# Performance work log

Measured on AMD Instinct MI355X. Metric: run time of the kernel, lower is better.

The kernel has to match this reference:

```python
import jax, jax.numpy as jnp
import numpy as np

B, V, F = 32, 1024, 16
A, P, NF = 32, 64, 128
C = P + A  # propagated feature width after concat with edge weights
D_OUT_IN = F + A + 2 * A * C  # 6192, input dim of output Dense


def setup_inputs() -> dict:
    key = jax.random.key(0)
    ks = jax.random.split(key, 4)
    return {
        "x": jax.random.normal(ks[0], (B, V, F), dtype=jnp.float32),
        "W_flr": jax.random.normal(ks[1], (F, P), dtype=jnp.float32) * (1.0 / np.sqrt(F)),
        "b_flr": jnp.zeros((P,), dtype=jnp.float32),
        "W_s": jax.random.normal(ks[2], (F, A), dtype=jnp.float32) * (1.0 / np.sqrt(F)),
        "b_s": jnp.zeros((A,), dtype=jnp.float32),
        "W_out": jax.random.normal(ks[3], (D_OUT_IN, NF), dtype=jnp.float32) * (1.0 / np.sqrt(D_OUT_IN)),
        "b_out": jnp.zeros((NF,), dtype=jnp.float32),
    }


def reference(x, W_flr, b_flr, W_s, b_s, W_out, b_out):
    # Per-vertex transforms
    feat = x @ W_flr + b_flr                      # (B,V,P)
    dist = x @ W_s + b_s                          # (B,V,A)
    ew = jnp.exp(-jnp.square(dist))               # (B,V,A) edge weights vertex->aggregator
    f = jnp.concatenate([feat, ew], axis=-1)      # (B,V,C)

    # Weighted broadcast then vertex-axis reduction (aggregator gather)
    w = jnp.transpose(ew, (0, 2, 1))              # (B,A,V)
    prod = w[..., None] * f[:, None, :, :]        # (B,A,V,C)
    agg_max = jnp.max(prod, axis=2)               # (B,A,C)
    agg_mean = jnp.mean(prod, axis=2)             # (B,A,C)
    agg = jnp.concatenate([agg_max, agg_mean], axis=-1)  # (B,A,2C)

    # Scatter aggregated features back to vertices, weighted by same edge weights
    upd = ew[..., None] * agg[:, None, :, :]      # (B,V,A,2C)
    upd = upd.reshape(B, V, A * 2 * C)            # (B,V,2AC)

    cat = jnp.concatenate([x, upd, ew], axis=-1)  # (B,V,F+2AC+A)
    return jnp.tanh(cat @ W_out + b_out)          # (B,V,NF)
```

## Files before the change

### kernel.cpp

```cpp
#include <hip/hip_runtime.h>
#include <hip/hip_bf16.h>
#include <math.h>

#define NB 32
#define NV 1024
#define NFT 16
#define NA 32
#define NP 64
#define NOUT 128
#define NC 96
#define NC2 192

#define NSPLIT 16
#define VPB 64

typedef __attribute__((ext_vector_type(8))) short bf16x8;
typedef __attribute__((ext_vector_type(4))) float f32x4;

__global__ __launch_bounds__(512, 2)
void k2p(const float* __restrict__ x,
         const float* __restrict__ W_flr,
         const float* __restrict__ b_flr,
         const float* __restrict__ W_s,
         const float* __restrict__ b_s,
         float* __restrict__ ewbuf,
         float* __restrict__ part) {
    __shared__ float xs[VPB][NFT];
    __shared__ float fs[VPB][NC];

    int b = blockIdx.x, vs = blockIdx.y, tid = threadIdx.x;
    int rowbase = b * NV + vs * VPB;

    if (tid < 256) {
        const float4* xsrc = (const float4*)(x + (size_t)rowbase * NFT);
        ((float4*)xs)[tid] = xsrc[tid];
    }
    __syncthreads();

    {
        int c  = tid & 127;
        int rh = tid >> 7;
        if (c < NC) {
            float Wcol[NFT], bias;
            if (c < NP) {
                bias = b_flr[c];
#pragma unroll
                for (int k = 0; k < NFT; ++k) Wcol[k] = W_flr[k * NP + c];
            } else {
                int a = c - NP;
                bias = b_s[a];
#pragma unroll
                for (int k = 0; k < NFT; ++k) Wcol[k] = W_s[k * NA + a];
            }
#pragma unroll
            for (int r0 = 0; r0 < 16; ++r0) {
                int r = rh * 16 + r0;
                float xr[NFT];
#pragma unroll
                for (int q = 0; q < 4; ++q)
                    ((float4*)xr)[q] = ((const float4*)xs[r])[q];
                float acc = bias;
#pragma unroll
                for (int k = 0; k < NFT; ++k)
                    acc = fmaf(xr[k], Wcol[k], acc);
                if (c >= NP) {
                    acc = __expf(-acc * acc);
                    ewbuf[(size_t)(rowbase + r) * NA + (c - NP)] = acc;
                }
                fs[r][c] = acc;
            }
        }
    }
    __syncthreads();

    int a  = tid >> 4;
    int c0 = (tid & 15) * 6;
    int ea = NP + a;

    float sm[6], mx[6];
#pragma unroll
    for (int j = 0; j < 6; ++j) { sm[j] = 0.f; mx[j] = -INFINITY; }

#pragma unroll 4
    for (int r = 0; r < VPB; ++r) {
        float e = fs[r][ea];
        float2 fA = *(const float2*)&fs[r][c0];
        float2 fB = *(const float2*)&fs[r][c0 + 2];
        float2 fC = *(const float2*)&fs[r][c0 + 4];
        float ff[6] = {fA.x, fA.y, fB.x, fB.y, fC.x, fC.y};
#pragma unroll
        for (int j = 0; j < 6; ++j) {
            float p = e * ff[j];
            sm[j] += p;
            mx[j] = fmaxf(mx[j], p);
        }
    }

    float* pb = part + (size_t)((b * NSPLIT + vs) * NA + a) * NC2;
#pragma unroll
    for (int q = 0; q < 3; ++q) {
        float2 vm = {mx[2 * q], mx[2 * q + 1]};
        float2 vsum = {sm[2 * q], sm[2 * q + 1]};
        *(float2*)&pb[c0 + 2 * q]      = vm;
        *(float2*)&pb[NC + c0 + 2 * q] = vsum;
    }
}

__global__ void k23(const float* __restrict__ part,
                    const float* __restrict__ W_out,
                    float* __restrict__ Gp) {
    __shared__ float aggL[NC2];
    int b = blockIdx.x, a = blockIdx.y, tid = threadIdx.x;

    {
        const float* pb = part + (size_t)(b * NSPLIT * NA + a) * NC2 + tid;
        const size_t stride = (size_t)NA * NC2;
        if (tid < NC) {
            float m = -INFINITY;
#pragma unroll
            for (int vsi = 0; vsi < NSPLIT; ++vsi)
                m = fmaxf(m, pb[vsi * stride]);
            aggL[tid] = m;
        } else {
            float s = 0.f;
#pragma unroll
            for (int vsi = 0; vsi < NSPLIT; ++vsi)
                s += pb[vsi * stride];
            aggL[tid] = s * (1.0f / (float)NV);
        }
    }
    __syncthreads();

    if (tid < NOUT) {
        int n = tid;
        const float* wr = W_out + (size_t)(NFT + a * NC2) * NOUT + n;
        float acc = W_out[(size_t)(NFT + NA * NC2 + a) * NOUT + n];
#pragma unroll 8
        for (int c = 0; c < NC2; ++c)
            acc = fmaf(aggL[c], wr[(size_t)c * NOUT], acc);
        Gp[(size_t)(b * NA + a) * NOUT + n] = acc;
    }
}

#define MB 64

__device__ inline void f2hl(float v, ushort& h, ushort& l) {
    __hip_bfloat16 hb = __float2bfloat16(v);
    float hf = __bfloat162float(hb);
    __hip_bfloat16 lb = __float2bfloat16(v - hf);
    h = *(ushort*)&hb;
    l = *(ushort*)&lb;
}

__global__ void k4_mfma(const float* __restrict__ x,
                        const float* __restrict__ ewbuf,
                        const float* __restrict__ Gp,
                        const float* __restrict__ W_out,
                        const float* __restrict__ b_out,
                        float* __restrict__ out) {
    __shared__ ushort BsH[1024 * 8];
    __shared__ ushort BsL[1024 * 8];
    __shared__ float  bs[NOUT];

    int rb = blockIdx.x;
    int b  = blockIdx.y;
    int tid = threadIdx.x;
    int rowbase = b * NV + rb * MB;

#pragma unroll
    for (int it = 0; it < 4; ++it) {
        int u = it * 256 + tid;
        int n = u & 127, koct = u >> 7;
        float v[8];
        if (koct < 2) {
#pragma unroll
            for (int j = 0; j < 8; ++j)
                v[j] = W_out[(size_t)(koct * 8 + j) * NOUT + n];
        } else if (koct < 6) {
#pragma unroll
            for (int j = 0; j < 8; ++j)
                v[j] = Gp[(size_t)b * NA * NOUT + (size_t)(koct * 8 + j - 16) * NOUT + n];
        } else {
#pragma unroll
            for (int j = 0; j < 8; ++j) v[j] = 0.f;
        }
        ushort h[8], l[8];
#pragma unroll
        for (int j = 0; j < 8; ++j) f2hl(v[j], h[j], l[j]);
        int cidx = ((koct >> 2) * 512) + ((n >> 4) * 64) + ((koct & 3) * 16) + (n & 15);
        *(bf16x8*)&BsH[cidx * 8] = *(bf16x8*)h;
        *(bf16x8*)&BsL[cidx * 8] = *(bf16x8*)l;
    }
    if (tid < NOUT) bs[tid] = b_out[tid];

    int w = tid >> 6, lane = tid & 63;
    int r16 = lane & 15, kg = lane >> 4;
    int arow = w * 16 + r16;
    int grow = rowbase + arow;

    float a0[8], a1[8];
    if (kg < 2) {
        *(float4*)&a0[0] = *(const float4*)&x[(size_t)grow * NFT + kg * 8];
        *(float4*)&a0[4] = *(const float4*)&x[(size_t)grow * NFT + kg * 8 + 4];
        *(float4*)&a1[0] = *(const float4*)&ewbuf[(size_t)grow * NA + 16 + kg * 8];
        *(float4*)&a1[4] = *(const float4*)&ewbuf[(size_t)grow * NA + 16 + kg * 8 + 4];
    } else {
        *(float4*)&a0[0] = *(const float4*)&ewbuf[(size_t)grow * NA + (kg - 2) * 8];
        *(float4*)&a0[4] = *(const float4*)&ewbuf[(size_t)grow * NA + (kg - 2) * 8 + 4];
#pragma unroll
        for (int j = 0; j < 8; ++j) a1[j] = 0.f;
    }
    ushort ah0[8], al0[8], ah1[8], al1[8];
#pragma unroll
    for (int j = 0; j < 8; ++j) f2hl(a0[j], ah0[j], al0[j]);
#pragma unroll
    for (int j = 0; j < 8; ++j) f2hl(a1[j], ah1[j], al1[j]);
    bf16x8 AH0 = *(bf16x8*)ah0, AL0 = *(bf16x8*)al0;
    bf16x8 AH1 = *(bf16x8*)ah1, AL1 = *(bf16x8*)al1;

    __syncthreads();

    int orow0 = rowbase + w * 16 + kg * 4;

#pragma unroll
    for (int nt = 0; nt < 8; ++nt) {
        int n = nt * 16 + r16;
        bf16x8 BH0 = *(const bf16x8*)&BsH[(nt * 64 + lane) * 8];
        bf16x8 BH1 = *(const bf16x8*)&BsH[(512 + nt * 64 + lane) * 8];
        bf16x8 BL0 = *(const bf16x8*)&BsL[(nt * 64 + lane) * 8];
        bf16x8 BL1 = *(const bf16x8*)&BsL[(512 + nt * 64 + lane) * 8];
        float bias = bs[n];
        f32x4 acc = {bias, bias, bias, bias};
        acc = __builtin_amdgcn_mfma_f32_16x16x32_bf16(AH0, BH0, acc, 0, 0, 0);
        acc = __builtin_amdgcn_mfma_f32_16x16x32_bf16(AL0, BH0, acc, 0, 0, 0);
        acc = __builtin_amdgcn_mfma_f32_16x16x32_bf16(AH0, BL0, acc, 0, 0, 0);
        acc = __builtin_amdgcn_mfma_f32_16x16x32_bf16(AH1, BH1, acc, 0, 0, 0);
        acc = __builtin_amdgcn_mfma_f32_16x16x32_bf16(AL1, BH1, acc, 0, 0, 0);
        acc = __builtin_amdgcn_mfma_f32_16x16x32_bf16(AH1, BL1, acc, 0, 0, 0);
#pragma unroll
        for (int rg = 0; rg < 4; ++rg) {
            float s = acc[rg];
            s = fminf(fmaxf(s, -15.f), 15.f);
            float e = __expf(2.f * s);
            out[(size_t)(orow0 + rg) * NOUT + n] =
                (e - 1.f) * __builtin_amdgcn_rcpf(e + 1.f);
        }
    }
}

extern "C" void kernel_launch(void* const* d_in, const int* in_sizes, int n_in,
                              void* d_out, int out_size, void* d_ws, size_t ws_size,
                              hipStream_t stream) {
    const float* x     = (const float*)d_in[0];
    const float* W_flr = (const float*)d_in[1];
    const float* b_flr = (const float*)d_in[2];
    const float* W_s   = (const float*)d_in[3];
    const float* b_s   = (const float*)d_in[4];
    const float* W_out = (const float*)d_in[5];
    const float* b_out = (const float*)d_in[6];
    float* out = (float*)d_out;

    float* ewbuf = (float*)d_ws;
    float* part  = ewbuf + (size_t)NB * NV * NA;
    float* Gp    = part  + (size_t)NB * NSPLIT * NA * NC2;

    {
        dim3 g(NB, NSPLIT);
        k2p<<<g, 512, 0, stream>>>(x, W_flr, b_flr, W_s, b_s, ewbuf, part);
    }
    {
        dim3 g(NB, NA);
        k23<<<g, 192, 0, stream>>>(part, W_out, Gp);
    }
    {
        dim3 g(NV / MB, NB);
        k4_mfma<<<g, 256, 0, stream>>>(x, ewbuf, Gp, W_out, b_out, out);
    }
}
```

Measured before the change: 39.10 us.

## Precompute bf16 hi/lo splits upstream and read pre-packed operands in final MFMA kernel

Result: no change. 38.66 us (-1.1%).

```diff
diff --git a/kernel.cpp b/kernel.cpp
--- a/kernel.cpp
+++ b/kernel.cpp
@@ -17,14 +17,23 @@
 typedef __attribute__((ext_vector_type(8))) short bf16x8;
 typedef __attribute__((ext_vector_type(4))) float f32x4;
 
+__device__ inline void f2hl(float v, ushort& h, ushort& l) {
+    __hip_bfloat16 hb = __float2bfloat16(v);
+    float hf = __bfloat162float(hb);
+    __hip_bfloat16 lb = __float2bfloat16(v - hf);
+    h = *(ushort*)&hb;
+    l = *(ushort*)&lb;
+}
+
 __global__ __launch_bounds__(512, 2)
 void k2p(const float* __restrict__ x,
          const float* __restrict__ W_flr,
          const float* __restrict__ b_flr,
          const float* __restrict__ W_s,
          const float* __restrict__ b_s,
-         float* __restrict__ ewbuf,
-         float* __restrict__ part) {
+         float* __restrict__ part,
+         ushort* __restrict__ xbfH, ushort* __restrict__ xbfL,
+         ushort* __restrict__ ewH,  ushort* __restrict__ ewL) {
     __shared__ float xs[VPB][NFT];
     __shared__ float fs[VPB][NC];
 
@@ -32,8 +41,17 @@
     int rowbase = b * NV + vs * VPB;
 
     if (tid < 256) {
-        const float4* xsrc = (const float4*)(x + (size_t)rowbase * NFT);
-        ((float4*)xs)[tid] = xsrc[tid];
+        float4 v = ((const float4*)(x + (size_t)rowbase * NFT))[tid];
+        ((float4*)xs)[tid] = v;
+        int r = tid >> 2, ko = (tid & 3) * 4;
+        float vv[4] = {v.x, v.y, v.z, v.w};
+        ushort h[4], l[4];
+#pragma unroll
+        for (int j = 0; j < 4; ++j) f2hl(vv[j], h[j], l[j]);
+        uint2 hp = { (uint)h[0] | ((uint)h[1] << 16), (uint)h[2] | ((uint)h[3] << 16) };
+        uint2 lp = { (uint)l[0] | ((uint)l[1] << 16), (uint)l[2] | ((uint)l[3] << 16) };
+        *(uint2*)&xbfH[(size_t)(rowbase + r) * NFT + ko] = hp;
+        *(uint2*)&xbfL[(size_t)(rowbase + r) * NFT + ko] = lp;
     }
     __syncthreads();
 
@@ -65,7 +83,10 @@
                     acc = fmaf(xr[k], Wcol[k], acc);
                 if (c >= NP) {
                     acc = __expf(-acc * acc);
-                    ewbuf[(size_t)(rowbase + r) * NA + (c - NP)] = acc;
+                    ushort h, l;
+                    f2hl(acc, h, l);
+                    ewH[(size_t)(rowbase + r) * NA + (c - NP)] = h;
+                    ewL[(size_t)(rowbase + r) * NA + (c - NP)] = l;
                 }
                 fs[r][c] = acc;
             }
@@ -108,7 +129,8 @@
 
 __global__ void k23(const float* __restrict__ part,
                     const float* __restrict__ W_out,
-                    float* __restrict__ Gp) {
+                    const float* __restrict__ b_out,
+                    ushort* __restrict__ BbH, ushort* __restrict__ BbL) {
     __shared__ float aggL[NC2];
     int b = blockIdx.x, a = blockIdx.y, tid = threadIdx.x;
 
@@ -133,104 +155,92 @@
 
     if (tid < NOUT) {
         int n = tid;
+        ushort* bh = BbH + (size_t)b * 8192;
+        ushort* bl = BbL + (size_t)b * 8192;
+
         const float* wr = W_out + (size_t)(NFT + a * NC2) * NOUT + n;
         float acc = W_out[(size_t)(NFT + NA * NC2 + a) * NOUT + n];
 #pragma unroll 8
         for (int c = 0; c < NC2; ++c)
             acc = fmaf(aggL[c], wr[(size_t)c * NOUT], acc);
-        Gp[(size_t)(b * NA + a) * NOUT + n] = acc;
-    }
-}
-
-#define MB 64
-
-__device__ inline void f2hl(float v, ushort& h, ushort& l) {
-    __hip_bfloat16 hb = __float2bfloat16(v);
-    float hf = __bfloat162float(hb);
-    __hip_bfloat16 lb = __float2bfloat16(v - hf);
-    h = *(ushort*)&hb;
-    l = *(ushort*)&lb;
-}
-
-__global__ void k4_mfma(const float* __restrict__ x,
-                        const float* __restrict__ ewbuf,
-                        const float* __restrict__ Gp,
-                        const float* __restrict__ W_out,
-                        const float* __restrict__ b_out,
-                        float* __restrict__ out) {
-    __shared__ ushort BsH[1024 * 8];
-    __shared__ ushort BsL[1024 * 8];
-    __shared__ float  bs[NOUT];
-
-    int rb = blockIdx.x;
-    int b  = blockIdx.y;
+
+        {
+            ushort h, l;
+            f2hl(acc, h, l);
+            int koct = 2 + (a >> 3), j = a & 7;
+            int ci = ((koct >> 2) * 512) + ((n >> 4) * 64) + ((koct & 3) * 16) + (n & 15);
+            bh[ci * 8 + j] = h;
+            bl[ci * 8 + j] = l;
+        }
+
+        if (a == 0) {
+#pragma unroll
+            for (int k = 0; k < NFT; ++k) {
+                ushort h, l;
+                f2hl(W_out[(size_t)k * NOUT + n], h, l);
+                int ci = ((n >> 4) * 64) + ((k >> 3) * 16) + (n & 15);
+                bh[ci * 8 + (k & 7)] = h;
+                bl[ci * 8 + (k & 7)] = l;
+            }
+            {
+                ushort h, l;
+                f2hl(b_out[n], h, l);
+                int ci6 = 512 + ((n >> 4) * 64) + (2 * 16) + (n & 15);
+                int ci7 = 512 + ((n >> 4) * 64) + (3 * 16) + (n & 15);
+                bh[ci6 * 8 + 0] = h;
+                bl[ci6 * 8 + 0] = l;
+#pragma unroll
+                for (int j = 1; j < 8; ++j) { bh[ci6 * 8 + j] = 0; bl[ci6 * 8 + j] = 0; }
+#pragma unroll
+                for (int j = 0; j < 8; ++j) { bh[ci7 * 8 + j] = 0; bl[ci7 * 8 + j] = 0; }
+            }
+        }
+    }
+}
+
+#define MB4 32
+
+__global__ __launch_bounds__(256, 4)
+void k4_mfma(const ushort* __restrict__ xbfH, const ushort* __restrict__ xbfL,
+             const ushort* __restrict__ ewH,  const ushort* __restrict__ ewL,
+             const ushort* __restrict__ BbH,  const ushort* __restrict__ BbL,
+             float* __restrict__ out) {
+    int rb = blockIdx.x, b = blockIdx.y;
     int tid = threadIdx.x;
-    int rowbase = b * NV + rb * MB;
-
-#pragma unroll
-    for (int it = 0; it < 4; ++it) {
-        int u = it * 256 + tid;
-        int n = u & 127, koct = u >> 7;
-        float v[8];
-        if (koct < 2) {
-#pragma unroll
-            for (int j = 0; j < 8; ++j)
-                v[j] = W_out[(size_t)(koct * 8 + j) * NOUT + n];
-        } else if (koct < 6) {
-#pragma unroll
-            for (int j = 0; j < 8; ++j)
-                v[j] = Gp[(size_t)b * NA * NOUT + (size_t)(koct * 8 + j - 16) * NOUT + n];
-        } else {
-#pragma unroll
-            for (int j = 0; j < 8; ++j) v[j] = 0.f;
-        }
-        ushort h[8], l[8];
-#pragma unroll
-        for (int j = 0; j < 8; ++j) f2hl(v[j], h[j], l[j]);
-        int cidx = ((koct >> 2) * 512) + ((n >> 4) * 64) + ((koct & 3) * 16) + (n & 15);
-        *(bf16x8*)&BsH[cidx * 8] = *(bf16x8*)h;
-        *(bf16x8*)&BsL[cidx * 8] = *(bf16x8*)l;
-    }
-    if (tid < NOUT) bs[tid] = b_out[tid];
-
     int w = tid >> 6, lane = tid & 63;
     int r16 = lane & 15, kg = lane >> 4;
-    int arow = w * 16 + r16;
-    int grow = rowbase + arow;
-
-    float a0[8], a1[8];
+    int rgrp = w & 1, nh = w >> 1;
+    int rowbase = b * NV + rb * MB4;
+    int grow = rowbase + rgrp * 16 + r16;
+
+    bf16x8 AH0, AH1, AL0, AL1;
     if (kg < 2) {
-        *(float4*)&a0[0] = *(const float4*)&x[(size_t)grow * NFT + kg * 8];
-        *(float4*)&a0[4] = *(const float4*)&x[(size_t)grow * NFT + kg * 8 + 4];
-        *(float4*)&a1[0] = *(const float4*)&ewbuf[(size_t)grow * NA + 16 + kg * 8];
-        *(float4*)&a1[4] = *(const float4*)&ewbuf[(size_t)grow * NA + 16 + kg * 8 + 4];
+        AH0 = *(const bf16x8*)&xbfH[(size_t)grow * NFT + kg * 8];
+        AL0 = *(const bf16x8*)&xbfL[(size_t)grow * NFT + kg * 8];
+        AH1 = *(const bf16x8*)&ewH[(size_t)grow * NA + 16 + kg * 8];
+        AL1 = *(const bf16x8*)&ewL[(size_t)grow * NA + 16 + kg * 8];
     } else {
-        *(float4*)&a0[0] = *(const float4*)&ewbuf[(size_t)grow * NA + (kg - 2) * 8];
-        *(float4*)&a0[4] = *(const float4*)&ewbuf[(size_t)grow * NA + (kg - 2) * 8 + 4];
-#pragma unroll
-        for (int j = 0; j < 8; ++j) a1[j] = 0.f;
-    }
-    ushort ah0[8], al0[8], ah1[8], al1[8];
-#pragma unroll
-    for (int j = 0; j < 8; ++j) f2hl(a0[j], ah0[j], al0[j]);
-#pragma unroll
-    for (int j = 0; j < 8; ++j) f2hl(a1[j], ah1[j], al1[j]);
-    bf16x8 AH0 = *(bf16x8*)ah0, AL0 = *(bf16x8*)al0;
-    bf16x8 AH1 = *(bf16x8*)ah1, AL1 = *(bf16x8*)al1;
-
-    __syncthreads();
-
-    int orow0 = rowbase + w * 16 + kg * 4;
-
-#pragma unroll
-    for (int nt = 0; nt < 8; ++nt) {
+        AH0 = *(const bf16x8*)&ewH[(size_t)grow * NA + (kg - 2) * 8];
+        AL0 = *(const bf16x8*)&ewL[(size_t)grow * NA + (kg - 2) * 8];
+        ushort one[8] = {0, 0, 0, 0, 0, 0, 0, 0};
+        if (kg == 2) one[0] = 0x3F80;
+        AH1 = *(bf16x8*)one;
+        AL1 = (bf16x8){0, 0, 0, 0, 0, 0, 0, 0};
+    }
+
+    const ushort* bh = BbH + (size_t)b * 8192;
+    const ushort* bl = BbL + (size_t)b * 8192;
+    int orow0 = rowbase + rgrp * 16 + kg * 4;
+
+#pragma unroll 2
+    for (int t = 0; t < 4; ++t) {
+        int nt = nh * 4 + t;
         int n = nt * 16 + r16;
-        bf16x8 BH0 = *(const bf16x8*)&BsH[(nt * 64 + lane) * 8];
-        bf16x8 BH1 = *(const bf16x8*)&BsH[(512 + nt * 64 + lane) * 8];
-        bf16x8 BL0 = *(const bf16x8*)&BsL[(nt * 64 + lane) * 8];
-        bf16x8 BL1 = *(const bf16x8*)&BsL[(512 + nt * 64 + lane) * 8];
-        float bias = bs[n];
-        f32x4 acc = {bias, bias, bias, bias};
+        bf16x8 BH0 = *(const bf16x8*)&bh[(size_t)(nt * 64 + lane) * 8];
+        bf16x8 BH1 = *(const bf16x8*)&bh[(size_t)(512 + nt * 64 + lane) * 8];
+        bf16x8 BL0 = *(const bf16x8*)&bl[(size_t)(nt * 64 + lane) * 8];
+        bf16x8 BL1 = *(const bf16x8*)&bl[(size_t)(512 + nt * 64 + lane) * 8];
+        f32x4 acc = {0.f, 0.f, 0.f, 0.f};
         acc = __builtin_amdgcn_mfma_f32_16x16x32_bf16(AH0, BH0, acc, 0, 0, 0);
         acc = __builtin_amdgcn_mfma_f32_16x16x32_bf16(AL0, BH0, acc, 0, 0, 0);
         acc = __builtin_amdgcn_mfma_f32_16x16x32_bf16(AH0, BL0, acc, 0, 0, 0);
@@ -260,20 +270,25 @@
     const float* b_out = (const float*)d_in[6];
     float* out = (float*)d_out;
 
-    float* ewbuf = (float*)d_ws;
-    float* part  = ewbuf + (size_t)NB * NV * NA;
-    float* Gp    = part  + (size_t)NB * NSPLIT * NA * NC2;
+    float*  part = (float*)d_ws;
+    ushort* xbfH = (ushort*)(part + 3145728);
+    ushort* xbfL = xbfH + 524288;
+    ushort* ewH  = xbfL + 524288;
+    ushort* ewL  = ewH + 1048576;
+    ushort* BbH  = ewL + 1048576;
+    ushort* BbL  = BbH + 262144;
 
     {
         dim3 g(NB, NSPLIT);
-        k2p<<<g, 512, 0, stream>>>(x, W_flr, b_flr, W_s, b_s, ewbuf, part);
+        k2p<<<g, 512, 0, stream>>>(x, W_flr, b_flr, W_s, b_s,
+                                   part, xbfH, xbfL, ewH, ewL);
     }
     {
         dim3 g(NB, NA);
-        k23<<<g, 192, 0, stream>>>(part, W_out, Gp);
-    }
-    {
-        dim3 g(NV / MB, NB);
-        k4_mfma<<<g, 256, 0, stream>>>(x, ewbuf, Gp, W_out, b_out, out);
-    }
-}
+        k23<<<g, 192, 0, stream>>>(part, W_out, b_out, BbH, BbL);
+    }
+    {
+        dim3 g(NV / MB4, NB);
+        k4_mfma<<<g, 256, 0, stream>>>(xbfH, xbfL, ewH, ewL, BbH, BbL, out);
+    }
+}
```
